# Kernel tuning notes

Hardware: AMD Instinct MI355X
Metric: run time of the kernel (lower is better)

## Reference

```python
import jax, jax.numpy as jnp
import numpy as np

NHEAD = 8
K_NEIGH = 16


def setup_inputs() -> dict:
    key = jax.random.key(0)
    ks = jax.random.split(key, 6)
    B, L, D = 4, 4096, 512
    x = jax.random.normal(ks[0], (B, L, D), dtype=jnp.float32)
    positions = jax.random.uniform(ks[1], (B, L, 3), dtype=jnp.float32)
    in_proj_w = jax.random.normal(ks[2], (3 * D, D), dtype=jnp.float32) * 0.02
    in_proj_b = jax.random.normal(ks[3], (3 * D,), dtype=jnp.float32) * 0.02
    out_proj_w = jax.random.normal(ks[4], (D, D), dtype=jnp.float32) * 0.02
    out_proj_b = jax.random.normal(ks[5], (D,), dtype=jnp.float32) * 0.02
    return {"x": x, "positions": positions, "in_proj_w": in_proj_w,
            "in_proj_b": in_proj_b, "out_proj_w": out_proj_w, "out_proj_b": out_proj_b}


def _sparse_attention(x, positions, in_proj_w, in_proj_b, out_proj_w, out_proj_b):
    B, L, D = x.shape
    H, dh = NHEAD, D // NHEAD
    K = min(K_NEIGH, L)
    scale = 1.0 / jnp.sqrt(jnp.asarray(dh, x.dtype))

    # Pairwise distances [B, L, L]; topk smallest -> neighbor indices [B, L, K].
    diff = positions[:, :, None, :] - positions[:, None, :, :]
    dist = jnp.sqrt(jnp.sum(diff * diff, axis=-1))
    _, nbr = jax.lax.top_k(-dist, K)  # [B, L, K]

    Wq, Wk, Wv = in_proj_w[:D], in_proj_w[D:2 * D], in_proj_w[2 * D:]
    bq, bk, bv = in_proj_b[:D], in_proj_b[D:2 * D], in_proj_b[2 * D:]

    # Query is x[b, i] itself (self is always its own nearest neighbor at dist 0),
    # so the selected attention row equals attention with query x[b, i] over neighbors.
    q = ((x @ Wq.T + bq) * scale).reshape(B, L, H, dh)

    # Gather neighbor features: [B, L, K, D]
    b_idx = jnp.arange(B)[:, None, None]
    local_x = x[b_idx, nbr]
    k = (local_x @ Wk.T + bk).reshape(B, L, K, H, dh)
    v = (local_x @ Wv.T + bv).reshape(B, L, K, H, dh)

    scores = jnp.einsum('blhd,blkhd->blhk', q, k)
    attn = jax.nn.softmax(scores, axis=-1)
    ctx = jnp.einsum('blhk,blkhd->blhd', attn, v).reshape(B, L, D)
    out = ctx @ out_proj_w.T + out_proj_b

    # Faithful fallback: if i not among its neighbors, pass through x[b, i].
    is_in = jnp.any(nbr == jnp.arange(L)[None, :, None], axis=-1)  # [B, L]
    return jnp.where(is_in[..., None], out, x)


def reference(x, positions, in_proj_w, in_proj_b, out_proj_w, out_proj_b):
    return _sparse_attention(x, positions, in_proj_w, in_proj_b, out_proj_w, out_proj_b)
```

## Files before the change

kernel.cpp:

```cpp
#include <hip/hip_runtime.h>
#include <cfloat>
#include <cmath>

constexpr int B = 4;
constexpr int L = 4096;
constexpr int D = 512;
constexpr int NH = 8;
constexpr int DH = 64;
constexpr int KN = 16;
constexpr int M = B * L;
constexpr int N_IN = 3 * D;
constexpr int NCELL = 512;

typedef __attribute__((ext_vector_type(8))) short short8;
typedef __attribute__((ext_vector_type(4))) float f32x4;
typedef unsigned short ushort;

__device__ __forceinline__ ushort f2bf(float f) {
  unsigned u = __float_as_uint(f);
  u = u + 0x7fffu + ((u >> 16) & 1u);
  return (ushort)(u >> 16);
}
__device__ __forceinline__ float bf2f(ushort h) {
  return __uint_as_float(((unsigned)h) << 16);
}
__device__ __forceinline__ float dot8(const uint4 qu, const uint4 ku, float a) {
  a = fmaf(bf2f((ushort)qu.x), bf2f((ushort)ku.x), a);
  a = fmaf(bf2f((ushort)(qu.x >> 16)), bf2f((ushort)(ku.x >> 16)), a);
  a = fmaf(bf2f((ushort)qu.y), bf2f((ushort)ku.y), a);
  a = fmaf(bf2f((ushort)(qu.y >> 16)), bf2f((ushort)(ku.y >> 16)), a);
  a = fmaf(bf2f((ushort)qu.z), bf2f((ushort)ku.z), a);
  a = fmaf(bf2f((ushort)(qu.z >> 16)), bf2f((ushort)(ku.z >> 16)), a);
  a = fmaf(bf2f((ushort)qu.w), bf2f((ushort)ku.w), a);
  a = fmaf(bf2f((ushort)(qu.w >> 16)), bf2f((ushort)(ku.w >> 16)), a);
  return a;
}
__device__ __forceinline__ uint2 pack4hi(const float4 v) {
  uint2 o;
  o.x = (unsigned)f2bf(v.x) | ((unsigned)f2bf(v.y) << 16);
  o.y = (unsigned)f2bf(v.z) | ((unsigned)f2bf(v.w) << 16);
  return o;
}
__device__ __forceinline__ void gload16(const void* g, void* l) {
  __builtin_amdgcn_global_load_lds(
      (const __attribute__((address_space(1))) void*)g,
      (__attribute__((address_space(3))) void*)l, 16, 0, 0);
}
__device__ __forceinline__ int morton3(int x, int y, int z) {
  int m = 0;
#pragma unroll
  for (int i = 0; i < 3; ++i)
    m |= (((x >> i) & 1) << (3 * i + 2)) | (((y >> i) & 1) << (3 * i + 1)) |
         (((z >> i) & 1) << (3 * i));
  return m;
}

__global__ __launch_bounds__(256) void cvt_x_kernel(const float* __restrict__ in,
                                                    ushort* __restrict__ out) {
  const int n8 = M * D / 8;
  for (int i = blockIdx.x * 256 + threadIdx.x; i < n8; i += gridDim.x * 256) {
    const float4 v0 = reinterpret_cast<const float4*>(in)[i * 2];
    const float4 v1 = reinterpret_cast<const float4*>(in)[i * 2 + 1];
    uint4 o;
    const uint2 a = pack4hi(v0), b2 = pack4hi(v1);
    o.x = a.x; o.y = a.y; o.z = b2.x; o.w = b2.y;
    reinterpret_cast<uint4*>(out)[i] = o;
  }
}

__global__ __launch_bounds__(256) void cvt_w_kernel(const float* __restrict__ in_w,
                                                    const float* __restrict__ out_w,
                                                    ushort* __restrict__ iwh,
                                                    ushort* __restrict__ owh,
                                                    ushort* __restrict__ owl) {
  const int ni8 = N_IN * D / 8;
  const int no8 = D * D / 8;
  for (int i = blockIdx.x * 256 + threadIdx.x; i < ni8 + no8; i += gridDim.x * 256) {
    if (i < ni8) {
      const float4 v0 = reinterpret_cast<const float4*>(in_w)[i * 2];
      const float4 v1 = reinterpret_cast<const float4*>(in_w)[i * 2 + 1];
      uint4 o;
      const uint2 a = pack4hi(v0), b2 = pack4hi(v1);
      o.x = a.x; o.y = a.y; o.z = b2.x; o.w = b2.y;
      reinterpret_cast<uint4*>(iwh)[i] = o;
    } else {
      const int j = i - ni8;
      const float4 v0 = reinterpret_cast<const float4*>(out_w)[j * 2];
      const float4 v1 = reinterpret_cast<const float4*>(out_w)[j * 2 + 1];
      uint4 oh, ol;
      const uint2 a = pack4hi(v0), b2 = pack4hi(v1);
      oh.x = a.x; oh.y = a.y; oh.z = b2.x; oh.w = b2.y;
      const float4 r0 = make_float4(v0.x - bf2f(f2bf(v0.x)), v0.y - bf2f(f2bf(v0.y)),
                                    v0.z - bf2f(f2bf(v0.z)), v0.w - bf2f(f2bf(v0.w)));
      const float4 r1 = make_float4(v1.x - bf2f(f2bf(v1.x)), v1.y - bf2f(f2bf(v1.y)),
                                    v1.z - bf2f(f2bf(v1.z)), v1.w - bf2f(f2bf(v1.w)));
      const uint2 c = pack4hi(r0), d2 = pack4hi(r1);
      ol.x = c.x; ol.y = c.y; ol.z = d2.x; ol.w = d2.y;
      reinterpret_cast<uint4*>(owh)[j] = oh;
      reinterpret_cast<uint4*>(owl)[j] = ol;
    }
  }
}

__global__ __launch_bounds__(256) void cell_rank_kernel(const float* __restrict__ pos,
                                                        int* __restrict__ cellOf,
                                                        int* __restrict__ rankOf,
                                                        int* __restrict__ hist) {
  const int i = blockIdx.x * 256 + threadIdx.x;
  if (i >= M) return;
  const float* p = pos + (size_t)i * 3;
  const int ix = min(7, max(0, (int)(p[0] * 8.f)));
  const int iy = min(7, max(0, (int)(p[1] * 8.f)));
  const int iz = min(7, max(0, (int)(p[2] * 8.f)));
  const int cell = morton3(ix, iy, iz);
  cellOf[i] = cell;
  rankOf[i] = atomicAdd(&hist[(i >> 12) * NCELL + cell], 1);
}

__global__ __launch_bounds__(512) void scan_kernel(const int* __restrict__ hist,
                                                   int* __restrict__ offs) {
  __shared__ int4 tmp[NCELL];
  const int t = threadIdx.x;
  const int4 v = make_int4(hist[0 * NCELL + t], hist[1 * NCELL + t],
                           hist[2 * NCELL + t], hist[3 * NCELL + t]);
  int4 acc = v;
  tmp[t] = acc;
  __syncthreads();
  for (int s = 1; s < NCELL; s <<= 1) {
    const int4 o = (t >= s) ? tmp[t - s] : make_int4(0, 0, 0, 0);
    __syncthreads();
    acc.x += o.x; acc.y += o.y; acc.z += o.z; acc.w += o.w;
    tmp[t] = acc;
    __syncthreads();
  }
  offs[0 * NCELL + t] = acc.x - v.x;
  offs[1 * NCELL + t] = acc.y - v.y;
  offs[2 * NCELL + t] = acc.z - v.z;
  offs[3 * NCELL + t] = acc.w - v.w;
}

__global__ __launch_bounds__(256) void scatter_kernel(const int* __restrict__ cellOf,
                                                      const int* __restrict__ rankOf,
                                                      const int* __restrict__ offs,
                                                      int* __restrict__ qorder) {
  const int i = blockIdx.x * 256 + threadIdx.x;
  if (i >= M) return;
  const int b = i >> 12;
  const int slot = offs[b * NCELL + cellOf[i]] + rankOf[i];
  qorder[b * L + slot] = i & (L - 1);
}

constexpr int TP = 65;

__global__ __launch_bounds__(512) void topk_kernel(const float* __restrict__ pos,
                                                   int* __restrict__ nbr,
                                                   int* __restrict__ isin) {
  __shared__ float sxT[64 * TP], syT[64 * TP], szT[64 * TP];
  __shared__ unsigned long long lst[8 * 64];
  const int wave = threadIdx.x >> 6;
  const int lane = threadIdx.x & 63;
  const int b = blockIdx.x >> 9;
  const int l = (blockIdx.x & 511) * 8 + wave;
  const int row = b * L + l;

  const float* p = pos + (size_t)b * L * 3;
  for (int i = threadIdx.x; i < L; i += 512) {
    const int a = (i & 63) * TP + (i >> 6);
    sxT[a] = p[3 * i + 0];
    syT[a] = p[3 * i + 1];
    szT[a] = p[3 * i + 2];
  }
  __syncthreads();

  const int qa = (l & 63) * TP + (l >> 6);
  const float qx = sxT[qa], qy = syT[qa], qz = szT[qa];

  float mA = FLT_MAX, mB2 = FLT_MAX, mC = FLT_MAX, mD2 = FLT_MAX;
  const int base = lane * TP;
  for (int j = 0; j < 64; j += 4) {
#define D2(t, acc)                                                   \
    {                                                                \
      const int a = base + j + t;                                    \
      const float dx = qx - sxT[a], dy = qy - syT[a], dz = qz - szT[a]; \
      acc = fminf(acc, fmaf(dx, dx, fmaf(dy, dy, dz * dz)));         \
    }
    D2(0, mA) D2(1, mB2) D2(2, mC) D2(3, mD2)
#undef D2
  }
  const unsigned mbits = __float_as_uint(fminf(fminf(mA, mB2), fminf(mC, mD2)));

  unsigned lo = 1, hi = 0x40400001u;
  while (lo < hi) {
    const unsigned mid = (lo + hi) >> 1;
    const int c = __popcll(__ballot(mbits < mid));
    if (c >= 16) hi = mid; else lo = mid + 1;
  }
  const unsigned P = lo + 16;

  int cnt = 0;
  unsigned long long am = __ballot(mbits < P);
  const unsigned long long below = (1ull << lane) - 1ull;
  while (am) {
    const int pl = (int)__builtin_ctzll(am);
    am &= am - 1;
    const int a = pl * TP + lane;
    const float dx = qx - sxT[a], dy = qy - syT[a], dz = qz - szT[a];
    const float d2 = fmaf(dx, dx, fmaf(dy, dy, dz * dz));
    const bool hit = __float_as_uint(d2) < P;
    const unsigned long long msk = __ballot(hit);
    if (hit) {
      const int slot = cnt + __popcll(msk & below);
      if (slot < 64) {
        const unsigned c = (unsigned)(lane * 64 + pl);
        lst[wave * 64 + slot] =
            ((unsigned long long)__float_as_uint(sqrtf(d2)) << 32) | c;
      }
    }
    cnt += __popcll(msk);
  }
  const int n = min(cnt, 64);

  const unsigned long long mine = (lane < n) ? lst[wave * 64 + lane] : ~0ull;
  int r = 0;
  for (int i = 0; i < n; ++i) r += (lst[wave * 64 + i] < mine) ? 1 : 0;

  const int idx = (int)(unsigned)(mine & 0xffffffffu);
  const bool wr = (lane < n) && (r < 16);
  if (wr) nbr[(size_t)row * KN + r] = idx;
  const unsigned long long hit2 = __ballot(wr && idx == l);
  if (lane == 0) isin[row] = hit2 ? 1 : 0;
}

constexpr int BM = 128, BN = 128, BK = 32;

__global__ __launch_bounds__(256) void gemm_in(const ushort* __restrict__ A,
                                               const ushort* __restrict__ W,
                                               const float* __restrict__ bias,
                                               ushort* __restrict__ qb,
                                               ushort* __restrict__ kb,
                                               ushort* __restrict__ vb) {
  __shared__ ushort Ah[BM * BK];
  __shared__ ushort Bh[BN * BK];

  const int tid = threadIdx.x;
  const int m0 = blockIdx.x * BM;
  const int n0 = blockIdx.y * BN;

  const int wv = tid >> 6;
  const int lane = tid & 63;
  const int sr = wv * 16 + (lane >> 2);
  const int sc = (lane & 3) * 8;
  const ushort* Asrc = A + (size_t)(m0 + sr) * D + sc;
  const ushort* Wsrc = W + (size_t)(n0 + sr) * D + sc;
  ushort* AhB0 = Ah + (wv * 16) * BK;
  ushort* AhB1 = Ah + (wv * 16 + 64) * BK;
  ushort* BhB0 = Bh + (wv * 16) * BK;
  ushort* BhB1 = Bh + (wv * 16 + 64) * BK;

  const int wr0 = (wv >> 1) * 64;
  const int wc0 = (wv & 1) * 64;
  const int fr_row = lane & 15;
  const int kof = (lane >> 4) * 8;

  f32x4 acc[4][4];
#pragma unroll
  for (int i = 0; i < 4; ++i)
#pragma unroll
    for (int j = 0; j < 4; ++j) acc[i][j] = {0.f, 0.f, 0.f, 0.f};

  for (int k0 = 0; k0 < D; k0 += BK) {
    __syncthreads();
    gload16(Asrc + k0, AhB0);
    gload16(Asrc + (size_t)64 * D + k0, AhB1);
    gload16(Wsrc + k0, BhB0);
    gload16(Wsrc + (size_t)64 * D + k0, BhB1);
    __syncthreads();

    short8 ah[4];
#pragma unroll
    for (int fr = 0; fr < 4; ++fr)
      ah[fr] = *reinterpret_cast<const short8*>(&Ah[(wr0 + fr * 16 + fr_row) * BK + kof]);
#pragma unroll
    for (int fc = 0; fc < 4; ++fc) {
      const short8 bh = *reinterpret_cast<const short8*>(&Bh[(wc0 + fc * 16 + fr_row) * BK + kof]);
#pragma unroll
      for (int fr = 0; fr < 4; ++fr)
        acc[fr][fc] = __builtin_amdgcn_mfma_f32_16x16x32_bf16(ah[fr], bh, acc[fr][fc], 0, 0, 0);
    }
  }

  const int region = n0 >> 9;
  ushort* outb = region == 0 ? qb : (region == 1 ? kb : vb);
  const float scl = region == 0 ? 0.125f : 1.0f;
  const int nloc0 = (n0 & 511) + wc0;
#pragma unroll
  for (int fr = 0; fr < 4; ++fr) {
#pragma unroll
    for (int r = 0; r < 4; ++r) {
      const int grow = m0 + wr0 + fr * 16 + (lane >> 4) * 4 + r;
#pragma unroll
      for (int fc = 0; fc < 4; ++fc) {
        const int cc = fc * 16 + (lane & 15);
        const float v = (acc[fr][fc][r] + bias[n0 + wc0 + cc]) * scl;
        outb[(size_t)grow * D + nloc0 + cc] = f2bf(v);
      }
    }
  }
}

__global__ __launch_bounds__(256) void gemm_out(const ushort* __restrict__ A,
                                                const ushort* __restrict__ Wh,
                                                const ushort* __restrict__ Wl,
                                                const float* __restrict__ bias,
                                                float* __restrict__ C,
                                                const float* __restrict__ X,
                                                const int* __restrict__ isin) {
  __shared__ ushort Ah[BM * BK];
  __shared__ ushort Bh[BN * BK];
  __shared__ ushort Bl[BN * BK];

  const int tid = threadIdx.x;
  const int m0 = blockIdx.x * BM;
  const int n0 = blockIdx.y * BN;

  const int wv = tid >> 6;
  const int lane = tid & 63;
  const int sr = wv * 16 + (lane >> 2);
  const int sc = (lane & 3) * 8;
  const ushort* Asrc = A + (size_t)(m0 + sr) * D + sc;
  const ushort* Hsrc = Wh + (size_t)(n0 + sr) * D + sc;
  const ushort* Lsrc = Wl + (size_t)(n0 + sr) * D + sc;
  ushort* AhB0 = Ah + (wv * 16) * BK;
  ushort* AhB1 = Ah + (wv * 16 + 64) * BK;
  ushort* BhB0 = Bh + (wv * 16) * BK;
  ushort* BhB1 = Bh + (wv * 16 + 64) * BK;
  ushort* BlB0 = Bl + (wv * 16) * BK;
  ushort* BlB1 = Bl + (wv * 16 + 64) * BK;

  const int wr0 = (wv >> 1) * 64;
  const int wc0 = (wv & 1) * 64;
  const int fr_row = lane & 15;
  const int kof = (lane >> 4) * 8;

  f32x4 acc[4][4];
#pragma unroll
  for (int i = 0; i < 4; ++i)
#pragma unroll
    for (int j = 0; j < 4; ++j) acc[i][j] = {0.f, 0.f, 0.f, 0.f};

  for (int k0 = 0; k0 < D; k0 += BK) {
    __syncthreads();
    gload16(Asrc + k0, AhB0);
    gload16(Asrc + (size_t)64 * D + k0, AhB1);
    gload16(Hsrc + k0, BhB0);
    gload16(Hsrc + (size_t)64 * D + k0, BhB1);
    gload16(Lsrc + k0, BlB0);
    gload16(Lsrc + (size_t)64 * D + k0, BlB1);
    __syncthreads();

    short8 ah[4];
#pragma unroll
    for (int fr = 0; fr < 4; ++fr)
      ah[fr] = *reinterpret_cast<const short8*>(&Ah[(wr0 + fr * 16 + fr_row) * BK + kof]);
#pragma unroll
    for (int fc = 0; fc < 4; ++fc) {
      const short8 bh = *reinterpret_cast<const short8*>(&Bh[(wc0 + fc * 16 + fr_row) * BK + kof]);
      const short8 bl = *reinterpret_cast<const short8*>(&Bl[(wc0 + fc * 16 + fr_row) * BK + kof]);
#pragma unroll
      for (int fr = 0; fr < 4; ++fr) {
        acc[fr][fc] = __builtin_amdgcn_mfma_f32_16x16x32_bf16(ah[fr], bh, acc[fr][fc], 0, 0, 0);
        acc[fr][fc] = __builtin_amdgcn_mfma_f32_16x16x32_bf16(ah[fr], bl, acc[fr][fc], 0, 0, 0);
      }
    }
  }

#pragma unroll
  for (int fr = 0; fr < 4; ++fr) {
#pragma unroll
    for (int r = 0; r < 4; ++r) {
      const int grow = m0 + wr0 + fr * 16 + (lane >> 4) * 4 + r;
      const int ok = isin[grow];
#pragma unroll
      for (int fc = 0; fc < 4; ++fc) {
        const int gcol = n0 + wc0 + fc * 16 + (lane & 15);
        float v = acc[fr][fc][r] + bias[gcol];
        if (!ok) v = X[(size_t)grow * D + gcol];
        C[(size_t)grow * D + gcol] = v;
      }
    }
  }
}

__global__ __launch_bounds__(256) void attn_kernel(const ushort* __restrict__ qb,
                                                   const ushort* __restrict__ kb,
                                                   const ushort* __restrict__ vb,
                                                   const int* __restrict__ nbr,
                                                   const int* __restrict__ qorder,
                                                   ushort* __restrict__ ctx) {
  const int wave = threadIdx.x >> 6;
  const int lane = threadIdx.x & 63;
  const int xcd = blockIdx.x & 7;
  const int chunk = blockIdx.x >> 3;
  const int b = xcd >> 1;
  const int slot = ((xcd & 1) * 512 + chunk) * 4 + wave;
  const int l = qorder[b * L + slot];
  const int bl = b * L + l;
  const int bbase = b * L;
  const int* nb = nbr + (size_t)bl * KN;

  const int h = lane >> 3;
  const int n0 = lane & 7;
  const int glane = h * 8;

  const ushort* qp = qb + (size_t)bl * D + h * DH;
  uint4 qv[8];
#pragma unroll
  for (int i = 0; i < 8; ++i)
    qv[i] = *reinterpret_cast<const uint4*>(qp + i * 8);

  const int j0 = nb[n0];
  const int j1 = nb[n0 + 8];
  float a0 = 0.f, a1 = 0.f;
  {
    const ushort* kr = kb + (size_t)(bbase + j0) * D + h * DH;
#pragma unroll
    for (int i = 0; i < 8; ++i)
      a0 = dot8(qv[i], *reinterpret_cast<const uint4*>(kr + i * 8), a0);
  }
  {
    const ushort* kr = kb + (size_t)(bbase + j1) * D + h * DH;
#pragma unroll
    for (int i = 0; i < 8; ++i)
      a1 = dot8(qv[i], *reinterpret_cast<const uint4*>(kr + i * 8), a1);
  }

  float mx = fmaxf(a0, a1);
  mx = fmaxf(mx, __shfl_xor(mx, 1));
  mx = fmaxf(mx, __shfl_xor(mx, 2));
  mx = fmaxf(mx, __shfl_xor(mx, 4));
  const float e0 = expf(a0 - mx), e1 = expf(a1 - mx);
  float sm = e0 + e1;
  sm += __shfl_xor(sm, 1);
  sm += __shfl_xor(sm, 2);
  sm += __shfl_xor(sm, 4);
  const float inv = 1.0f / sm;
  const float w0 = e0 * inv, w1 = e1 * inv;

  const int d0 = n0 * 8;
  float acc[8];
#pragma unroll
  for (int i = 0; i < 8; ++i) acc[i] = 0.f;
#pragma unroll
  for (int n = 0; n < KN; ++n) {
    const int src = glane + (n & 7);
    const float w = __shfl((n < 8) ? w0 : w1, src);
    const int j = __shfl((n < 8) ? j0 : j1, src);
    const uint4 vv = *reinterpret_cast<const uint4*>(
        vb + (size_t)(bbase + j) * D + h * DH + d0);
    acc[0] = fmaf(w, bf2f((ushort)vv.x), acc[0]);
    acc[1] = fmaf(w, bf2f((ushort)(vv.x >> 16)), acc[1]);
    acc[2] = fmaf(w, bf2f((ushort)vv.y), acc[2]);
    acc[3] = fmaf(w, bf2f((ushort)(vv.y >> 16)), acc[3]);
    acc[4] = fmaf(w, bf2f((ushort)vv.z), acc[4]);
    acc[5] = fmaf(w, bf2f((ushort)(vv.z >> 16)), acc[5]);
    acc[6] = fmaf(w, bf2f((ushort)vv.w), acc[6]);
    acc[7] = fmaf(w, bf2f((ushort)(vv.w >> 16)), acc[7]);
  }
  uint4 o;
  o.x = (unsigned)f2bf(acc[0]) | ((unsigned)f2bf(acc[1]) << 16);
  o.y = (unsigned)f2bf(acc[2]) | ((unsigned)f2bf(acc[3]) << 16);
  o.z = (unsigned)f2bf(acc[4]) | ((unsigned)f2bf(acc[5]) << 16);
  o.w = (unsigned)f2bf(acc[6]) | ((unsigned)f2bf(acc[7]) << 16);
  *reinterpret_cast<uint4*>(ctx + (size_t)bl * D + h * DH + d0) = o;
}

extern "C" void kernel_launch(void* const* d_in, const int* in_sizes, int n_in,
                              void* d_out, int out_size, void* d_ws, size_t ws_size,
                              hipStream_t stream) {
  const float* x     = (const float*)d_in[0];
  const float* pos   = (const float*)d_in[1];
  const float* in_w  = (const float*)d_in[2];
  const float* in_b  = (const float*)d_in[3];
  const float* out_w = (const float*)d_in[4];
  const float* out_b = (const float*)d_in[5];
  float* out = (float*)d_out;

  const size_t nbr_bytes  = (size_t)M * KN * sizeof(int);
  const size_t isin_bytes = (size_t)M * sizeof(int);
  const size_t half_bytes = (size_t)M * D * sizeof(ushort);
  const size_t iwh_bytes  = (size_t)N_IN * D * sizeof(ushort);
  const size_t ow_bytes   = (size_t)D * D * sizeof(ushort);
  const size_t sort_bytes = (size_t)M * sizeof(int);
  const size_t hist_bytes = (size_t)B * NCELL * sizeof(int);
  const size_t need = nbr_bytes + isin_bytes + 5 * half_bytes +
                      iwh_bytes + 2 * ow_bytes + 4 * sort_bytes +
                      2 * hist_bytes + 16384;
  if (ws_size < need) return;

  char* w = (char*)d_ws;
  int*    nbr    = (int*)w;    w += (nbr_bytes + 255) & ~(size_t)255;
  int*    isin   = (int*)w;    w += (isin_bytes + 255) & ~(size_t)255;
  ushort* xb     = (ushort*)w; w += (half_bytes + 255) & ~(size_t)255;
  ushort* qb     = (ushort*)w; w += (half_bytes + 255) & ~(size_t)255;
  ushort* kb     = (ushort*)w; w += (half_bytes + 255) & ~(size_t)255;
  ushort* vb     = (ushort*)w; w += (half_bytes + 255) & ~(size_t)255;
  ushort* ctxb   = (ushort*)w; w += (half_bytes + 255) & ~(size_t)255;
  ushort* iwh    = (ushort*)w; w += (iwh_bytes + 255) & ~(size_t)255;
  ushort* owh    = (ushort*)w; w += (ow_bytes + 255) & ~(size_t)255;
  ushort* owl    = (ushort*)w; w += (ow_bytes + 255) & ~(size_t)255;
  int*    cellOf = (int*)w;    w += (sort_bytes + 255) & ~(size_t)255;
  int*    rankOf = (int*)w;    w += (sort_bytes + 255) & ~(size_t)255;
  int*    qorder = (int*)w;    w += (sort_bytes + 255) & ~(size_t)255;
  int*    hist   = (int*)w;    w += (hist_bytes + 255) & ~(size_t)255;
  int*    offs   = (int*)w;

  cvt_x_kernel<<<2048, 256, 0, stream>>>(x, xb);
  cvt_w_kernel<<<512, 256, 0, stream>>>(in_w, out_w, iwh, owh, owl);

  hipMemsetAsync(hist, 0, hist_bytes, stream);
  cell_rank_kernel<<<M / 256, 256, 0, stream>>>(pos, cellOf, rankOf, hist);
  scan_kernel<<<1, NCELL, 0, stream>>>(hist, offs);
  scatter_kernel<<<M / 256, 256, 0, stream>>>(cellOf, rankOf, offs, qorder);

  topk_kernel<<<B * (L / 8), 512, 0, stream>>>(pos, nbr, isin);

  gemm_in<<<dim3(M / BM, N_IN / BN), 256, 0, stream>>>(xb, iwh, in_b, qb, kb, vb);

  attn_kernel<<<M / 4, 256, 0, stream>>>(qb, kb, vb, nbr, qorder, ctxb);

  gemm_out<<<dim3(M / BM, D / BN), 256, 0, stream>>>(ctxb, owh, owl, out_b, out, x, isin);
}
```

Measured before the change: 179.4 us.

## Fuse cell sort into one per-batch kernel and batch attention loads

Replaces the memset, cell/rank, scan and scatter kernels with a single per-batch kernel that builds the cell histogram in LDS with shared atomics, scans it, and scatters query order directly. This removes three launches, a memset and the global intermediate arrays. In the attention kernel, the two K dot products are interleaved, and the V gather is restructured to shuffle all weights and indices up front and then issue four loads at a time, exposing more memory-level parallelism at the cost of extra registers. The sort now runs on only four blocks, so it has very little parallelism.

```diff
diff --git a/kernel.cpp b/kernel.cpp
--- a/kernel.cpp
+++ b/kernel.cpp
@@ -34,6 +34,16 @@
   a = fmaf(bf2f((ushort)qu.w), bf2f((ushort)ku.w), a);
   a = fmaf(bf2f((ushort)(qu.w >> 16)), bf2f((ushort)(ku.w >> 16)), a);
   return a;
+}
+__device__ __forceinline__ void acc8(float wgt, const uint4 vv, float (&acc)[8]) {
+  acc[0] = fmaf(wgt, bf2f((ushort)vv.x), acc[0]);
+  acc[1] = fmaf(wgt, bf2f((ushort)(vv.x >> 16)), acc[1]);
+  acc[2] = fmaf(wgt, bf2f((ushort)vv.y), acc[2]);
+  acc[3] = fmaf(wgt, bf2f((ushort)(vv.y >> 16)), acc[3]);
+  acc[4] = fmaf(wgt, bf2f((ushort)vv.z), acc[4]);
+  acc[5] = fmaf(wgt, bf2f((ushort)(vv.z >> 16)), acc[5]);
+  acc[6] = fmaf(wgt, bf2f((ushort)vv.w), acc[6]);
+  acc[7] = fmaf(wgt, bf2f((ushort)(vv.w >> 16)), acc[7]);
 }
 __device__ __forceinline__ uint2 pack4hi(const float4 v) {
   uint2 o;
@@ -102,52 +112,47 @@
   }
 }
 
-__global__ __launch_bounds__(256) void cell_rank_kernel(const float* __restrict__ pos,
-                                                        int* __restrict__ cellOf,
-                                                        int* __restrict__ rankOf,
-                                                        int* __restrict__ hist) {
-  const int i = blockIdx.x * 256 + threadIdx.x;
-  if (i >= M) return;
-  const float* p = pos + (size_t)i * 3;
-  const int ix = min(7, max(0, (int)(p[0] * 8.f)));
-  const int iy = min(7, max(0, (int)(p[1] * 8.f)));
-  const int iz = min(7, max(0, (int)(p[2] * 8.f)));
-  const int cell = morton3(ix, iy, iz);
-  cellOf[i] = cell;
-  rankOf[i] = atomicAdd(&hist[(i >> 12) * NCELL + cell], 1);
-}
-
-__global__ __launch_bounds__(512) void scan_kernel(const int* __restrict__ hist,
-                                                   int* __restrict__ offs) {
-  __shared__ int4 tmp[NCELL];
+__global__ __launch_bounds__(512) void sort_kernel(const float* __restrict__ pos,
+                                                   int* __restrict__ qorder) {
+  __shared__ int hist[NCELL];
+  __shared__ int scanbuf[NCELL];
+  const int b = blockIdx.x;
   const int t = threadIdx.x;
-  const int4 v = make_int4(hist[0 * NCELL + t], hist[1 * NCELL + t],
-                           hist[2 * NCELL + t], hist[3 * NCELL + t]);
-  int4 acc = v;
-  tmp[t] = acc;
+  hist[t] = 0;
+  __syncthreads();
+
+  int cells[8], ranks[8];
+  const float* p = pos + (size_t)b * L * 3;
+#pragma unroll
+  for (int q = 0; q < 8; ++q) {
+    const int i = q * 512 + t;
+    const int ix = min(7, max(0, (int)(p[3 * i + 0] * 8.f)));
+    const int iy = min(7, max(0, (int)(p[3 * i + 1] * 8.f)));
+    const int iz = min(7, max(0, (int)(p[3 * i + 2] * 8.f)));
+    cells[q] = morton3(ix, iy, iz);
+    ranks[q] = atomicAdd(&hist[cells[q]], 1);
+  }
+  __syncthreads();
+
+  int accv = hist[t];
+  const int orig = accv;
+  scanbuf[t] = accv;
   __syncthreads();
   for (int s = 1; s < NCELL; s <<= 1) {
-    const int4 o = (t >= s) ? tmp[t - s] : make_int4(0, 0, 0, 0);
+    const int o = (t >= s) ? scanbuf[t - s] : 0;
     __syncthreads();
-    acc.x += o.x; acc.y += o.y; acc.z += o.z; acc.w += o.w;
-    tmp[t] = acc;
+    accv += o;
+    scanbuf[t] = accv;
     __syncthreads();
   }
-  offs[0 * NCELL + t] = acc.x - v.x;
-  offs[1 * NCELL + t] = acc.y - v.y;
-  offs[2 * NCELL + t] = acc.z - v.z;
-  offs[3 * NCELL + t] = acc.w - v.w;
-}
-
-__global__ __launch_bounds__(256) void scatter_kernel(const int* __restrict__ cellOf,
-                                                      const int* __restrict__ rankOf,
-                                                      const int* __restrict__ offs,
-                                                      int* __restrict__ qorder) {
-  const int i = blockIdx.x * 256 + threadIdx.x;
-  if (i >= M) return;
-  const int b = i >> 12;
-  const int slot = offs[b * NCELL + cellOf[i]] + rankOf[i];
-  qorder[b * L + slot] = i & (L - 1);
+  hist[t] = accv - orig;
+  __syncthreads();
+
+#pragma unroll
+  for (int q = 0; q < 8; ++q) {
+    const int i = q * 512 + t;
+    qorder[b * L + hist[cells[q]] + ranks[q]] = i;
+  }
 }
 
 constexpr int TP = 65;
@@ -422,16 +427,13 @@
   const int j1 = nb[n0 + 8];
   float a0 = 0.f, a1 = 0.f;
   {
-    const ushort* kr = kb + (size_t)(bbase + j0) * D + h * DH;
-#pragma unroll
-    for (int i = 0; i < 8; ++i)
-      a0 = dot8(qv[i], *reinterpret_cast<const uint4*>(kr + i * 8), a0);
-  }
-  {
-    const ushort* kr = kb + (size_t)(bbase + j1) * D + h * DH;
-#pragma unroll
-    for (int i = 0; i < 8; ++i)
-      a1 = dot8(qv[i], *reinterpret_cast<const uint4*>(kr + i * 8), a1);
+    const ushort* kr0 = kb + (size_t)(bbase + j0) * D + h * DH;
+    const ushort* kr1 = kb + (size_t)(bbase + j1) * D + h * DH;
+#pragma unroll
+    for (int i = 0; i < 8; ++i) {
+      a0 = dot8(qv[i], *reinterpret_cast<const uint4*>(kr0 + i * 8), a0);
+      a1 = dot8(qv[i], *reinterpret_cast<const uint4*>(kr1 + i * 8), a1);
+    }
   }
 
   float mx = fmaxf(a0, a1);
@@ -446,26 +448,33 @@
   const float inv = 1.0f / sm;
   const float w0 = e0 * inv, w1 = e1 * inv;
 
-  const int d0 = n0 * 8;
-  float acc[8];
-#pragma unroll
-  for (int i = 0; i < 8; ++i) acc[i] = 0.f;
+  float ww[KN];
+  int jj[KN];
 #pragma unroll
   for (int n = 0; n < KN; ++n) {
     const int src = glane + (n & 7);
-    const float w = __shfl((n < 8) ? w0 : w1, src);
-    const int j = __shfl((n < 8) ? j0 : j1, src);
-    const uint4 vv = *reinterpret_cast<const uint4*>(
-        vb + (size_t)(bbase + j) * D + h * DH + d0);
-    acc[0] = fmaf(w, bf2f((ushort)vv.x), acc[0]);
-    acc[1] = fmaf(w, bf2f((ushort)(vv.x >> 16)), acc[1]);
-    acc[2] = fmaf(w, bf2f((ushort)vv.y), acc[2]);
-    acc[3] = fmaf(w, bf2f((ushort)(vv.y >> 16)), acc[3]);
-    acc[4] = fmaf(w, bf2f((ushort)vv.z), acc[4]);
-    acc[5] = fmaf(w, bf2f((ushort)(vv.z >> 16)), acc[5]);
-    acc[6] = fmaf(w, bf2f((ushort)vv.w), acc[6]);
-    acc[7] = fmaf(w, bf2f((ushort)(vv.w >> 16)), acc[7]);
-  }
+    ww[n] = __shfl((n < 8) ? w0 : w1, src);
+    jj[n] = __shfl((n < 8) ? j0 : j1, src);
+  }
+
+  const int d0 = n0 * 8;
+  const ushort* vbase = vb + (size_t)bbase * D + h * DH + d0;
+  float acc[8];
+#pragma unroll
+  for (int i = 0; i < 8; ++i) acc[i] = 0.f;
+
+#pragma unroll
+  for (int g = 0; g < KN; g += 4) {
+    const uint4 va0 = *reinterpret_cast<const uint4*>(vbase + (size_t)jj[g] * D);
+    const uint4 va1 = *reinterpret_cast<const uint4*>(vbase + (size_t)jj[g + 1] * D);
+    const uint4 va2 = *reinterpret_cast<const uint4*>(vbase + (size_t)jj[g + 2] * D);
+    const uint4 va3 = *reinterpret_cast<const uint4*>(vbase + (size_t)jj[g + 3] * D);
+    acc8(ww[g], va0, acc);
+    acc8(ww[g + 1], va1, acc);
+    acc8(ww[g + 2], va2, acc);
+    acc8(ww[g + 3], va3, acc);
+  }
+
   uint4 o;
   o.x = (unsigned)f2bf(acc[0]) | ((unsigned)f2bf(acc[1]) << 16);
   o.y = (unsigned)f2bf(acc[2]) | ((unsigned)f2bf(acc[3]) << 16);
@@ -491,10 +500,8 @@
   const size_t iwh_bytes  = (size_t)N_IN * D * sizeof(ushort);
   const size_t ow_bytes   = (size_t)D * D * sizeof(ushort);
   const size_t sort_bytes = (size_t)M * sizeof(int);
-  const size_t hist_bytes = (size_t)B * NCELL * sizeof(int);
   const size_t need = nbr_bytes + isin_bytes + 5 * half_bytes +
-                      iwh_bytes + 2 * ow_bytes + 4 * sort_bytes +
-                      2 * hist_bytes + 16384;
+                      iwh_bytes + 2 * ow_bytes + sort_bytes + 16384;
   if (ws_size < need) return;
 
   char* w = (char*)d_ws;
@@ -508,19 +515,12 @@
   ushort* iwh    = (ushort*)w; w += (iwh_bytes + 255) & ~(size_t)255;
   ushort* owh    = (ushort*)w; w += (ow_bytes + 255) & ~(size_t)255;
   ushort* owl    = (ushort*)w; w += (ow_bytes + 255) & ~(size_t)255;
-  int*    cellOf = (int*)w;    w += (sort_bytes + 255) & ~(size_t)255;
-  int*    rankOf = (int*)w;    w += (sort_bytes + 255) & ~(size_t)255;
-  int*    qorder = (int*)w;    w += (sort_bytes + 255) & ~(size_t)255;
-  int*    hist   = (int*)w;    w += (hist_bytes + 255) & ~(size_t)255;
-  int*    offs   = (int*)w;
+  int*    qorder = (int*)w;
 
   cvt_x_kernel<<<2048, 256, 0, stream>>>(x, xb);
   cvt_w_kernel<<<512, 256, 0, stream>>>(in_w, out_w, iwh, owh, owl);
 
-  hipMemsetAsync(hist, 0, hist_bytes, stream);
-  cell_rank_kernel<<<M / 256, 256, 0, stream>>>(pos, cellOf, rankOf, hist);
-  scan_kernel<<<1, NCELL, 0, stream>>>(hist, offs);
-  scatter_kernel<<<M / 256, 256, 0, stream>>>(cellOf, rankOf, offs, qorder);
+  sort_kernel<<<B, 512, 0, stream>>>(pos, qorder);
 
   topk_kernel<<<B * (L / 8), 512, 0, stream>>>(pos, nbr, isin);
 
```

Measured after the change: 172.7 us. -3.7%, faster.
